# Kernel tuning notes

Hardware: AMD Instinct MI355X
Metric: run time of the kernel (lower is better)

## Reference

```python
import jax, jax.numpy as jnp
import numpy as np

N_USERS = 4096
N_ITEMS = 4096
D = 64  # embedding_dim / out_features
N = N_USERS + N_ITEMS
ALPHA = 0.2  # LeakyReLU slope
NEG_INF = jnp.float32(-9e15)


def setup_inputs() -> dict:
    key = jax.random.key(0)
    ks = jax.random.split(key, 11)
    s = 0.05  # xavier-ish scale
    rn = lambda k, shape: jax.random.normal(k, shape, jnp.float32) * s
    adj = jax.random.randint(ks[0], (N, N), 0, 2, jnp.int32)
    return {
        "adj": adj,
        "user_emb": rn(ks[1], (N_USERS, D)),
        "item_emb": rn(ks[2], (N_ITEMS, D)),
        "W0_w": rn(ks[3], (D, D)), "W0_b": rn(ks[4], (D,)), "a0": rn(ks[5], (2 * D, 1)),
        "W1_w": rn(ks[6], (D, D)), "W1_b": rn(ks[7], (D,)), "a1": rn(ks[8], (2 * D, 1)),
        "out_w": rn(ks[9], (D, D)), "out_b": rn(ks[10], (D,)),
    }


def gat_layer(x, adj, W_w, W_b, a):
    # Wh: [N, D]
    Wh = x @ W_w.T + W_b
    # Original materializes [N,N,2D] concat then matmul with a.
    # Algebraically identical: e_ij = leakyrelu(a1 . Wh_i + a2 . Wh_j)
    src = Wh @ a[:D]          # [N, 1] -> row contribution
    dst = (Wh @ a[D:]).T      # [1, N] -> column contribution
    e = jax.nn.leaky_relu(src + dst, ALPHA)        # [N, N]
    e = jnp.where(adj > 0, e, NEG_INF)
    att = jax.nn.softmax(e, axis=1)                # dropout=0.0 (eval)
    return att @ Wh                                 # [N, D]


def reference(adj, user_emb, item_emb, W0_w, W0_b, a0, W1_w, W1_b, a1, out_w, out_b):
    x = jnp.concatenate([user_emb, item_emb], axis=0)  # [N, D]
    x = jax.nn.relu(gat_layer(x, adj, W0_w, W0_b, a0))
    x = jax.nn.relu(gat_layer(x, adj, W1_w, W1_b, a1))
    u, it = x[:N_USERS], x[N_USERS:]
    return (u @ out_w.T + out_b, it @ out_w.T + out_b)
```

## Files before the change

### kernel.cpp

```cpp
#include <hip/hip_runtime.h>


typedef _Float16 f16x8 __attribute__((ext_vector_type(8)));
typedef _Float16 f16x2 __attribute__((ext_vector_type(2)));
typedef __attribute__((ext_vector_type(4))) float f32x4;

union Frag16 {
    f16x8        v;
    unsigned int u[4];
};
union HV2 {
    f16x2        v;
    _Float16     h[2];
    unsigned int u;
};

__global__ __launch_bounds__(256) void k_pack(
    const int* __restrict__ adj, unsigned long long* __restrict__ bits)
{
    int wgid = blockIdx.x * 4 + (threadIdx.x >> 6);
    int lane = threadIdx.x & 63;
    const long long NW  = 2048LL * 4;
    const long long TOT = 8192LL * 8192;
    for (long long base = (long long)wgid * 512; base < TOT; base += NW * 512) {
        int a[8];
#pragma unroll
        for (int i = 0; i < 8; i++) a[i] = adj[base + i * 64 + lane];
        unsigned long long m[8];
#pragma unroll
        for (int i = 0; i < 8; i++) m[i] = __ballot(a[i] != 0);
        if (lane < 4) {
            reinterpret_cast<ulonglong2*>(bits + (base >> 6))[lane] =
                ulonglong2{m[2 * lane], m[2 * lane + 1]};
        }
    }
}

__device__ __forceinline__ void prep_tail(
    float (*xs)[65], float (*Wt)[65], float (*sred)[64], float (*dred)[64],
    const float* __restrict__ W, const float* __restrict__ bias,
    const float* __restrict__ avec,
    _Float16* __restrict__ WhT,
    unsigned int* __restrict__ E12,
    _Float16* __restrict__ F1h, _Float16* __restrict__ F2h,
    int tid, int r0)
{
    for (int e = tid; e < 4096; e += 256) {
        int o = e >> 6, c = e & 63;
        Wt[c][o] = W[e];
    }
    __syncthreads();

    int r = tid & 63, chunk = tid >> 6, c0 = chunk * 16;
    float acc[16];
#pragma unroll
    for (int o = 0; o < 16; o++) acc[o] = bias[c0 + o];
    for (int c = 0; c < 64; c++) {
        float xv = xs[r][c];
#pragma unroll
        for (int o = 0; o < 16; o++) acc[o] += xv * Wt[c][c0 + o];
    }

    float sp = 0.f, dp = 0.f;
#pragma unroll
    for (int o = 0; o < 16; o++) {
        sp += acc[o] * avec[c0 + o];
        dp += acc[o] * avec[64 + c0 + o];
    }
    sred[chunk][r] = sp;
    dred[chunk][r] = dp;

#pragma unroll
    for (int o = 0; o < 16; o++)
        WhT[(size_t)(c0 + o) * 8192 + r0 + r] = (_Float16)acc[o];

    __syncthreads();
    if (tid < 64) {
        int g = r0 + tid;
        float s = sred[0][tid] + sred[1][tid] + sred[2][tid] + sred[3][tid];
        float d = dred[0][tid] + dred[1][tid] + dred[2][tid] + dred[3][tid];
        HV2 e;
        e.h[0] = (_Float16)__expf(s);
        e.h[1] = (_Float16)__expf(0.2f * s);
        E12[g] = e.u;
        F1h[g] = (_Float16)__expf(d);
        F2h[g] = (_Float16)__expf(0.2f * d);
    }
}

__global__ __launch_bounds__(256) void k_prep0(
    const float* __restrict__ ue, const float* __restrict__ ie,
    const float* __restrict__ W, const float* __restrict__ bias,
    const float* __restrict__ avec,
    _Float16* __restrict__ WhT, unsigned int* __restrict__ E12,
    _Float16* __restrict__ F1h, _Float16* __restrict__ F2h)
{
    __shared__ float xs[64][65];
    __shared__ float Wt[64][65];
    __shared__ float sred[4][64];
    __shared__ float dred[4][64];
    int tid = threadIdx.x, r0 = blockIdx.x * 64;

    for (int e = tid; e < 4096; e += 256) {
        int r = e >> 6, c = e & 63;
        int row = r0 + r;
        xs[r][c] = (row < 4096) ? ue[row * 64 + c] : ie[(row - 4096) * 64 + c];
    }
    prep_tail(xs, Wt, sred, dred, W, bias, avec, WhT, E12, F1h, F2h, tid, r0);
}

template <int NS>
__global__ __launch_bounds__(256) void k_prep1(
    const float* __restrict__ numP, const float* __restrict__ denP,
    const float* __restrict__ W, const float* __restrict__ bias,
    const float* __restrict__ avec,
    _Float16* __restrict__ WhT, unsigned int* __restrict__ E12,
    _Float16* __restrict__ F1h, _Float16* __restrict__ F2h)
{
    __shared__ float xs[64][65];
    __shared__ float Wt[64][65];
    __shared__ float sred[4][64];
    __shared__ float dred[4][64];
    __shared__ float dtot[64];
    int tid = threadIdx.x, r0 = blockIdx.x * 64;
    int rowblk = blockIdx.x;

    if (tid < 64) {
        float s = 0.f;
#pragma unroll
        for (int p = 0; p < NS; p++) s += denP[p * 8192 + r0 + tid];
        dtot[tid] = fmaxf(s, 1e-20f);
    }
    __syncthreads();
    for (int e = tid; e < 4096; e += 256) {
        int r = e >> 6;
        float s = 0.f;
#pragma unroll
        for (int p = 0; p < NS; p++)
            s += numP[(size_t)(p * 128 + rowblk) * 4096 + e];
        float v = s / dtot[r];
        xs[r][e & 63] = v > 0.f ? v : 0.f;
    }
    prep_tail(xs, Wt, sred, dred, W, bias, avec, WhT, E12, F1h, F2h, tid, r0);
}

struct AggSmem {
    union {
        _Float16 WhB[64][138];
        struct {
            float T[64][68];
            float denT[64];
        } ep;
    } u;
    unsigned int mkAll[64][20];
    unsigned int f1All[256];
    unsigned int f2All[256];
};

__device__ __forceinline__ void agg_body(
    const unsigned int* __restrict__ bits,
    const _Float16* __restrict__ WhT, const unsigned int* __restrict__ E12,
    const _Float16* __restrict__ F1h, const _Float16* __restrict__ F2h,
    float* __restrict__ numP, float* __restrict__ denP)
{
    constexpr int CK = 128, NCH = 4;
    __shared__ AggSmem sm;

    int tid  = threadIdx.x;
    int wave = tid >> 6, lane = tid & 63;
    int quad = lane >> 4, l16 = lane & 15;
    int rowblk = blockIdx.x, ks = blockIdx.y;
    int k0 = ks * (CK * NCH);

    {
        int row_l = tid >> 2, w4 = (tid & 3) * 4;
        uint4 v = *reinterpret_cast<const uint4*>(
            bits + (size_t)(rowblk * 64 + row_l) * 256 + ks * 16 + w4);
        *reinterpret_cast<uint4*>(&sm.mkAll[row_l][w4]) = v;
    }
    if (tid < 64) {
        uint4 v = *reinterpret_cast<const uint4*>(F1h + k0 + tid * 8);
        *reinterpret_cast<uint4*>(&sm.f1All[tid * 4]) = v;
    } else if (tid < 128) {
        int t2 = tid - 64;
        uint4 v = *reinterpret_cast<const uint4*>(F2h + k0 + t2 * 8);
        *reinterpret_cast<uint4*>(&sm.f2All[t2 * 4]) = v;
    }

    uint4 P[4];
#pragma unroll
    for (int i = 0; i < 4; i++) {
        int p = tid + 256 * i, f = p >> 4, c8 = (p & 15) * 8;
        P[i] = *reinterpret_cast<const uint4*>(WhT + (size_t)f * 8192 + k0 + c8);
    }
#pragma unroll
    for (int i = 0; i < 4; i++) {
        int p = tid + 256 * i, f = p >> 4, c8 = (p & 15) * 8;
        *reinterpret_cast<uint4*>(&sm.u.WhB[f][c8]) = P[i];
    }
    __syncthreads();

    int row = rowblk * 64 + wave * 16 + l16;
    int lrow = wave * 16 + l16;
    unsigned int e12 = E12[row];
    HV2 e1p, e2p;
    e1p.u = (e12 & 0xFFFFu);  e1p.u |= e1p.u << 16;
    e2p.u = (e12 >> 16);      e2p.u |= e2p.u << 16;

    f32x4 accs[4];
    f32x4 accd = {0.f, 0.f, 0.f, 0.f};
#pragma unroll
    for (int nt = 0; nt < 4; nt++) accs[nt] = accd;

    Frag16 ones;
    ones.u[0] = ones.u[1] = ones.u[2] = ones.u[3] = 0x3C003C00u;

    for (int c = 0; c < NCH; c++) {
        if (c + 1 < NCH) {
            int kc = k0 + (c + 1) * CK;
#pragma unroll
            for (int i = 0; i < 4; i++) {
                int p = tid + 256 * i, f = p >> 4, c8 = (p & 15) * 8;
                P[i] = *reinterpret_cast<const uint4*>(
                    WhT + (size_t)f * 8192 + kc + c8);
            }
        }

#pragma unroll
        for (int kb = 0; kb < CK; kb += 32) {
            int kq = kb + quad * 8;
            unsigned int word = sm.mkAll[lrow][c * 4 + (kb >> 5)];
            unsigned int w8 = word >> (quad * 8);

            int fidx = (c * CK + kq) >> 1;
            uint4 f1v = *reinterpret_cast<const uint4*>(&sm.f1All[fidx]);
            uint4 f2v = *reinterpret_cast<const uint4*>(&sm.f2All[fidx]);
            unsigned int f1a[4] = {f1v.x, f1v.y, f1v.z, f1v.w};
            unsigned int f2a[4] = {f2v.x, f2v.y, f2v.z, f2v.w};

            Frag16 A;
#pragma unroll
            for (int p = 0; p < 4; p++) {
                HV2 fa, fb, wa;
                fa.u = f1a[p];
                fb.u = f2a[p];
                wa.v = __builtin_elementwise_max(e1p.v * fa.v, e2p.v * fb.v);
                int s0 = ((int)(w8 << (31 - 2 * p))) >> 31;
                int s1 = ((int)(w8 << (30 - 2 * p))) >> 31;
                unsigned int pm = ((unsigned)s0 & 0xFFFFu) | ((unsigned)s1 << 16);
                A.u[p] = wa.u & pm;
            }

#pragma unroll
            for (int nt = 0; nt < 4; nt++) {
                Frag16 B;
                B.v = *reinterpret_cast<const f16x8*>(&sm.u.WhB[nt * 16 + l16][kq]);
                accs[nt] = __builtin_amdgcn_mfma_f32_16x16x32_f16(A.v, B.v,
                                                                  accs[nt], 0, 0, 0);
            }
            accd = __builtin_amdgcn_mfma_f32_16x16x32_f16(A.v, ones.v, accd, 0, 0, 0);
        }

        if (c + 1 < NCH) {
            __syncthreads();
#pragma unroll
            for (int i = 0; i < 4; i++) {
                int p = tid + 256 * i, f = p >> 4, c8 = (p & 15) * 8;
                *reinterpret_cast<uint4*>(&sm.u.WhB[f][c8]) = P[i];
            }
            __syncthreads();
        }
    }

    __syncthreads();
#pragma unroll
    for (int rr = 0; rr < 4; rr++) {
        int r = wave * 16 + quad * 4 + rr;
#pragma unroll
        for (int nt = 0; nt < 4; nt++)
            sm.u.ep.T[r][nt * 16 + l16] = accs[nt][rr];
        if (l16 == 0) sm.u.ep.denT[r] = accd[rr];
    }
    __syncthreads();

    float* dst = numP + (size_t)(ks * 128 + rowblk) * 4096;
#pragma unroll
    for (int i = 0; i < 4; i++) {
        int idx = i * 1024 + tid * 4;
        int r = idx >> 6, c2 = idx & 63;
        float4 v = *reinterpret_cast<const float4*>(&sm.u.ep.T[r][c2]);
        *reinterpret_cast<float4*>(dst + idx) = v;
    }
    if (tid < 64)
        denP[ks * 8192 + rowblk * 64 + tid] = sm.u.ep.denT[tid];
}

__global__ __launch_bounds__(256) void k_agg_l0(
    const unsigned int* __restrict__ bits,
    const _Float16* __restrict__ WhT, const unsigned int* __restrict__ E12,
    const _Float16* __restrict__ F1h, const _Float16* __restrict__ F2h,
    float* __restrict__ numP, float* __restrict__ denP)
{
    agg_body(bits, WhT, E12, F1h, F2h, numP, denP);
}

__global__ __launch_bounds__(256) void k_agg_l1(
    const unsigned int* __restrict__ bits,
    const _Float16* __restrict__ WhT, const unsigned int* __restrict__ E12,
    const _Float16* __restrict__ F1h, const _Float16* __restrict__ F2h,
    float* __restrict__ numP, float* __restrict__ denP)
{
    agg_body(bits, WhT, E12, F1h, F2h, numP, denP);
}

template <int NS>
__global__ __launch_bounds__(256) void k_out(
    const float* __restrict__ numP, const float* __restrict__ denP,
    const float* __restrict__ W, const float* __restrict__ bias,
    float* __restrict__ out)
{
    __shared__ float xs[64][65];
    __shared__ float Wt[64][65];
    __shared__ float dtot[64];
    int tid = threadIdx.x, r0 = blockIdx.x * 64;
    int rowblk = blockIdx.x;

    if (tid < 64) {
        float s = 0.f;
#pragma unroll
        for (int p = 0; p < NS; p++) s += denP[p * 8192 + r0 + tid];
        dtot[tid] = fmaxf(s, 1e-20f);
    }
    __syncthreads();
    for (int e = tid; e < 4096; e += 256) {
        int r = e >> 6;
        float s = 0.f;
#pragma unroll
        for (int p = 0; p < NS; p++)
            s += numP[(size_t)(p * 128 + rowblk) * 4096 + e];
        float v = s / dtot[r];
        xs[r][e & 63] = v > 0.f ? v : 0.f;
    }
    for (int e = tid; e < 4096; e += 256) {
        int o = e >> 6, c = e & 63;
        Wt[c][o] = W[e];
    }
    __syncthreads();

    int r = tid & 63, chunk = tid >> 6, c0 = chunk * 16;
    float acc[16];
#pragma unroll
    for (int o = 0; o < 16; o++) acc[o] = bias[c0 + o];
    for (int c = 0; c < 64; c++) {
        float xv = xs[r][c];
#pragma unroll
        for (int o = 0; o < 16; o++) acc[o] += xv * Wt[c][c0 + o];
    }
#pragma unroll
    for (int o = 0; o < 16; o++)
        out[(r0 + r) * 64 + c0 + o] = acc[o];
}

extern "C" void kernel_launch(void* const* d_in, const int* in_sizes, int n_in,
                              void* d_out, int out_size, void* d_ws, size_t ws_size,
                              hipStream_t stream)
{
    const int*   adj = (const int*)d_in[0];
    const float* ue  = (const float*)d_in[1];
    const float* ie  = (const float*)d_in[2];
    const float* W0w = (const float*)d_in[3];
    const float* W0b = (const float*)d_in[4];
    const float* a0  = (const float*)d_in[5];
    const float* W1w = (const float*)d_in[6];
    const float* W1b = (const float*)d_in[7];
    const float* a1  = (const float*)d_in[8];
    const float* Ow  = (const float*)d_in[9];
    const float* Ob  = (const float*)d_in[10];

    constexpr int NS = 16;

    char* ws = (char*)d_ws;
    size_t off = 0;
    auto alloc = [&](size_t bytes) -> char* {
        char* p = ws + off;
        off += (bytes + 255) & ~(size_t)255;
        return p;
    };
    float*        numP    = (float*)alloc((size_t)NS * 524288 * 4);
    float*        denP    = (float*)alloc((size_t)NS * 8192 * 4);
    unsigned long long* adjbits = (unsigned long long*)alloc(8192 * 1024);
    _Float16*     WhT0    = (_Float16*)alloc(64 * 8192 * 2);
    _Float16*     WhT1    = (_Float16*)alloc(64 * 8192 * 2);
    unsigned int* E12_0   = (unsigned int*)alloc(8192 * 4);
    unsigned int* E12_1   = (unsigned int*)alloc(8192 * 4);
    _Float16* F1h0 = (_Float16*)alloc(8192 * 2);
    _Float16* F2h0 = (_Float16*)alloc(8192 * 2);
    _Float16* F1h1 = (_Float16*)alloc(8192 * 2);
    _Float16* F2h1 = (_Float16*)alloc(8192 * 2);

    const unsigned int* bits32 = (const unsigned int*)adjbits;

    k_pack<<<2048, 256, 0, stream>>>(adj, adjbits);

    k_prep0<<<128, 256, 0, stream>>>(ue, ie, W0w, W0b, a0,
                                     WhT0, E12_0, F1h0, F2h0);
    k_agg_l0<<<dim3(128, NS), 256, 0, stream>>>(bits32, WhT0, E12_0,
                                                F1h0, F2h0, numP, denP);
    k_prep1<NS><<<128, 256, 0, stream>>>(numP, denP, W1w, W1b, a1,
                                         WhT1, E12_1, F1h1, F2h1);
    k_agg_l1<<<dim3(128, NS), 256, 0, stream>>>(bits32, WhT1, E12_1,
                                                F1h1, F2h1, numP, denP);
    k_out<NS><<<128, 256, 0, stream>>>(numP, denP, Ow, Ob, (float*)d_out);
}
```

Before: 511.0 us.

## Switch aggregation to 32x32x16 MFMA with 128-row blocks and swizzled LDS

The aggregation kernel now uses 32x32x16 f16 MFMA instead of 16x16x32. Each block covers 128 rows (32 per wave), so every generated attention A-fragment feeds larger MFMAs and the Wh tile is reused across twice as many rows. The Wh LDS tile uses an XOR-style rotated layout to avoid bank conflicts. The LDS-staged epilogue is replaced by direct per-lane stores, and the partial-sum layout and consumers are updated to match. The grid is halved (64x16 blocks), which reduces parallelism, and the direct scalar stores are less coalesced.

```diff
diff --git a/kernel.cpp b/kernel.cpp
--- a/kernel.cpp
+++ b/kernel.cpp
@@ -3,7 +3,7 @@
 
 typedef _Float16 f16x8 __attribute__((ext_vector_type(8)));
 typedef _Float16 f16x2 __attribute__((ext_vector_type(2)));
-typedef __attribute__((ext_vector_type(4))) float f32x4;
+typedef float    f32x16 __attribute__((ext_vector_type(16)));
 
 union Frag16 {
     f16x8        v;
@@ -123,7 +123,7 @@
     __shared__ float dred[4][64];
     __shared__ float dtot[64];
     int tid = threadIdx.x, r0 = blockIdx.x * 64;
-    int rowblk = blockIdx.x;
+    int rb128 = blockIdx.x >> 1, half = blockIdx.x & 1;
 
     if (tid < 64) {
         float s = 0.f;
@@ -137,7 +137,7 @@
         float s = 0.f;
 #pragma unroll
         for (int p = 0; p < NS; p++)
-            s += numP[(size_t)(p * 128 + rowblk) * 4096 + e];
+            s += numP[(size_t)(p * 64 + rb128) * 8192 + half * 4096 + e];
         float v = s / dtot[r];
         xs[r][e & 63] = v > 0.f ? v : 0.f;
     }
@@ -145,14 +145,8 @@
 }
 
 struct AggSmem {
-    union {
-        _Float16 WhB[64][138];
-        struct {
-            float T[64][68];
-            float denT[64];
-        } ep;
-    } u;
-    unsigned int mkAll[64][20];
+    uint4        WhBf[1024];
+    unsigned int mkAll[128][20];
     unsigned int f1All[256];
     unsigned int f2All[256];
 };
@@ -168,15 +162,17 @@
 
     int tid  = threadIdx.x;
     int wave = tid >> 6, lane = tid & 63;
-    int quad = lane >> 4, l16 = lane & 15;
+    int l32 = lane & 31, khalf = lane >> 5;
     int rowblk = blockIdx.x, ks = blockIdx.y;
     int k0 = ks * (CK * NCH);
 
-    {
-        int row_l = tid >> 2, w4 = (tid & 3) * 4;
+#pragma unroll
+    for (int j = 0; j < 2; j++) {
+        int s = tid + 256 * j;
+        int row_l = s >> 2, q = s & 3;
         uint4 v = *reinterpret_cast<const uint4*>(
-            bits + (size_t)(rowblk * 64 + row_l) * 256 + ks * 16 + w4);
-        *reinterpret_cast<uint4*>(&sm.mkAll[row_l][w4]) = v;
+            bits + (size_t)(rowblk * 128 + row_l) * 256 + ks * 16 + q * 4);
+        *reinterpret_cast<uint4*>(&sm.mkAll[row_l][q * 4]) = v;
     }
     if (tid < 64) {
         uint4 v = *reinterpret_cast<const uint4*>(F1h + k0 + tid * 8);
@@ -190,27 +186,24 @@
     uint4 P[4];
 #pragma unroll
     for (int i = 0; i < 4; i++) {
-        int p = tid + 256 * i, f = p >> 4, c8 = (p & 15) * 8;
-        P[i] = *reinterpret_cast<const uint4*>(WhT + (size_t)f * 8192 + k0 + c8);
+        int ff = (tid >> 3) + (i & 1) * 32, gg = (tid & 7) + (i >> 1) * 8;
+        P[i] = *reinterpret_cast<const uint4*>(WhT + (size_t)ff * 8192 + k0 + gg * 8);
     }
 #pragma unroll
     for (int i = 0; i < 4; i++) {
-        int p = tid + 256 * i, f = p >> 4, c8 = (p & 15) * 8;
-        *reinterpret_cast<uint4*>(&sm.u.WhB[f][c8]) = P[i];
-    }
-    __syncthreads();
-
-    int row = rowblk * 64 + wave * 16 + l16;
-    int lrow = wave * 16 + l16;
+        int ff = (tid >> 3) + (i & 1) * 32, gg = (tid & 7) + (i >> 1) * 8;
+        sm.WhBf[gg * 64 + ((ff + gg) & 63)] = P[i];
+    }
+    __syncthreads();
+
+    int row = rowblk * 128 + wave * 32 + l32;
+    int lrow = wave * 32 + l32;
     unsigned int e12 = E12[row];
     HV2 e1p, e2p;
     e1p.u = (e12 & 0xFFFFu);  e1p.u |= e1p.u << 16;
     e2p.u = (e12 >> 16);      e2p.u |= e2p.u << 16;
 
-    f32x4 accs[4];
-    f32x4 accd = {0.f, 0.f, 0.f, 0.f};
-#pragma unroll
-    for (int nt = 0; nt < 4; nt++) accs[nt] = accd;
+    f32x16 acc0 = {}, acc1 = {}, accd = {};
 
     Frag16 ones;
     ones.u[0] = ones.u[1] = ones.u[2] = ones.u[3] = 0x3C003C00u;
@@ -220,19 +213,19 @@
             int kc = k0 + (c + 1) * CK;
 #pragma unroll
             for (int i = 0; i < 4; i++) {
-                int p = tid + 256 * i, f = p >> 4, c8 = (p & 15) * 8;
+                int ff = (tid >> 3) + (i & 1) * 32, gg = (tid & 7) + (i >> 1) * 8;
                 P[i] = *reinterpret_cast<const uint4*>(
-                    WhT + (size_t)f * 8192 + kc + c8);
+                    WhT + (size_t)ff * 8192 + kc + gg * 8);
             }
         }
 
 #pragma unroll
-        for (int kb = 0; kb < CK; kb += 32) {
-            int kq = kb + quad * 8;
-            unsigned int word = sm.mkAll[lrow][c * 4 + (kb >> 5)];
-            unsigned int w8 = word >> (quad * 8);
-
-            int fidx = (c * CK + kq) >> 1;
+        for (int kb = 0; kb < CK; kb += 16) {
+            int wi = kb + khalf * 8;
+            unsigned int word = sm.mkAll[lrow][c * 4 + (wi >> 5)];
+            unsigned int w8 = word >> (wi & 31);
+
+            int fidx = (c * CK + wi) >> 1;
             uint4 f1v = *reinterpret_cast<const uint4*>(&sm.f1All[fidx]);
             uint4 f2v = *reinterpret_cast<const uint4*>(&sm.f2All[fidx]);
             unsigned int f1a[4] = {f1v.x, f1v.y, f1v.z, f1v.w};
@@ -251,48 +244,37 @@
                 A.u[p] = wa.u & pm;
             }
 
-#pragma unroll
-            for (int nt = 0; nt < 4; nt++) {
-                Frag16 B;
-                B.v = *reinterpret_cast<const f16x8*>(&sm.u.WhB[nt * 16 + l16][kq]);
-                accs[nt] = __builtin_amdgcn_mfma_f32_16x16x32_f16(A.v, B.v,
-                                                                  accs[nt], 0, 0, 0);
-            }
-            accd = __builtin_amdgcn_mfma_f32_16x16x32_f16(A.v, ones.v, accd, 0, 0, 0);
+            int g0 = (kb >> 3) + khalf;
+            Frag16 B0, B1;
+            B0.v = *reinterpret_cast<const f16x8*>(
+                &sm.WhBf[g0 * 64 + ((l32 + g0) & 63)]);
+            B1.v = *reinterpret_cast<const f16x8*>(
+                &sm.WhBf[g0 * 64 + ((32 + l32 + g0) & 63)]);
+            acc0 = __builtin_amdgcn_mfma_f32_32x32x16_f16(A.v, B0.v, acc0, 0, 0, 0);
+            acc1 = __builtin_amdgcn_mfma_f32_32x32x16_f16(A.v, B1.v, acc1, 0, 0, 0);
+            accd = __builtin_amdgcn_mfma_f32_32x32x16_f16(A.v, ones.v, accd, 0, 0, 0);
         }
 
         if (c + 1 < NCH) {
             __syncthreads();
 #pragma unroll
             for (int i = 0; i < 4; i++) {
-                int p = tid + 256 * i, f = p >> 4, c8 = (p & 15) * 8;
-                *reinterpret_cast<uint4*>(&sm.u.WhB[f][c8]) = P[i];
+                int ff = (tid >> 3) + (i & 1) * 32, gg = (tid & 7) + (i >> 1) * 8;
+                sm.WhBf[gg * 64 + ((ff + gg) & 63)] = P[i];
             }
             __syncthreads();
         }
     }
 
-    __syncthreads();
-#pragma unroll
-    for (int rr = 0; rr < 4; rr++) {
-        int r = wave * 16 + quad * 4 + rr;
-#pragma unroll
-        for (int nt = 0; nt < 4; nt++)
-            sm.u.ep.T[r][nt * 16 + l16] = accs[nt][rr];
-        if (l16 == 0) sm.u.ep.denT[r] = accd[rr];
-    }
-    __syncthreads();
-
-    float* dst = numP + (size_t)(ks * 128 + rowblk) * 4096;
-#pragma unroll
-    for (int i = 0; i < 4; i++) {
-        int idx = i * 1024 + tid * 4;
-        int r = idx >> 6, c2 = idx & 63;
-        float4 v = *reinterpret_cast<const float4*>(&sm.u.ep.T[r][c2]);
-        *reinterpret_cast<float4*>(dst + idx) = v;
-    }
-    if (tid < 64)
-        denP[ks * 8192 + rowblk * 64 + tid] = sm.u.ep.denT[tid];
+    float* tile = numP + (size_t)(ks * 64 + rowblk) * 8192;
+#pragma unroll
+    for (int r = 0; r < 16; r++) {
+        int rl = wave * 32 + (r & 3) + 8 * (r >> 2) + 4 * khalf;
+        tile[rl * 64 + l32]      = acc0[r];
+        tile[rl * 64 + 32 + l32] = acc1[r];
+        if (l32 == 0)
+            denP[ks * 8192 + rowblk * 128 + rl] = accd[r];
+    }
 }
 
 __global__ __launch_bounds__(256) void k_agg_l0(
@@ -323,7 +305,7 @@
     __shared__ float Wt[64][65];
     __shared__ float dtot[64];
     int tid = threadIdx.x, r0 = blockIdx.x * 64;
-    int rowblk = blockIdx.x;
+    int rb128 = blockIdx.x >> 1, half = blockIdx.x & 1;
 
     if (tid < 64) {
         float s = 0.f;
@@ -337,7 +319,7 @@
         float s = 0.f;
 #pragma unroll
         for (int p = 0; p < NS; p++)
-            s += numP[(size_t)(p * 128 + rowblk) * 4096 + e];
+            s += numP[(size_t)(p * 64 + rb128) * 8192 + half * 4096 + e];
         float v = s / dtot[r];
         xs[r][e & 63] = v > 0.f ? v : 0.f;
     }
@@ -386,7 +368,7 @@
         off += (bytes + 255) & ~(size_t)255;
         return p;
     };
-    float*        numP    = (float*)alloc((size_t)NS * 524288 * 4);
+    float*        numP    = (float*)alloc((size_t)NS * 64 * 8192 * 4);
     float*        denP    = (float*)alloc((size_t)NS * 8192 * 4);
     unsigned long long* adjbits = (unsigned long long*)alloc(8192 * 1024);
     _Float16*     WhT0    = (_Float16*)alloc(64 * 8192 * 2);
@@ -404,11 +386,11 @@
 
     k_prep0<<<128, 256, 0, stream>>>(ue, ie, W0w, W0b, a0,
                                      WhT0, E12_0, F1h0, F2h0);
-    k_agg_l0<<<dim3(128, NS), 256, 0, stream>>>(bits32, WhT0, E12_0,
-                                                F1h0, F2h0, numP, denP);
+    k_agg_l0<<<dim3(64, NS), 256, 0, stream>>>(bits32, WhT0, E12_0,
+                                               F1h0, F2h0, numP, denP);
     k_prep1<NS><<<128, 256, 0, stream>>>(numP, denP, W1w, W1b, a1,
                                          WhT1, E12_1, F1h1, F2h1);
-    k_agg_l1<<<dim3(128, NS), 256, 0, stream>>>(bits32, WhT1, E12_1,
-                                                F1h1, F2h1, numP, denP);
+    k_agg_l1<<<dim3(64, NS), 256, 0, stream>>>(bits32, WhT1, E12_1,
+                                               F1h1, F2h1, numP, denP);
     k_out<NS><<<128, 256, 0, stream>>>(numP, denP, Ow, Ob, (float*)d_out);
 }
```

Measured after the change: 477.2 us. 1.07x faster.
